# Optimization experiments

Hardware: AMD Instinct MI355X
Metric: run time of the kernel (lower is better)

Reference implementation:

```python
import jax, jax.numpy as jnp
import numpy as np

D_MODEL = 1024
NUM_HEADS = 16
HEAD_DIM = D_MODEL // NUM_HEADS


def setup_inputs() -> dict:
    key = jax.random.key(0)
    k_x, k_wqkv, k_bqkv, k_wout, k_bout = jax.random.split(key, 5)
    B, S = 2, 2048
    x = jax.random.normal(k_x, (B, S, D_MODEL), dtype=jnp.float32)
    # haiku Linear: y = x @ W + b, W shape [in, out]
    init_scale = 1.0 / np.sqrt(D_MODEL)
    W_qkv = jax.random.normal(k_wqkv, (D_MODEL, 3 * D_MODEL), dtype=jnp.float32) * init_scale
    b_qkv = jnp.zeros((3 * D_MODEL,), dtype=jnp.float32)
    W_out = jax.random.normal(k_wout, (D_MODEL, D_MODEL), dtype=jnp.float32) * init_scale
    b_out = jnp.zeros((D_MODEL,), dtype=jnp.float32)
    return {"x": x, "W_qkv": W_qkv, "b_qkv": b_qkv, "W_out": W_out, "b_out": b_out}


def reference(x, W_qkv, b_qkv, W_out, b_out):
    B, S, _ = x.shape
    qkv = x @ W_qkv + b_qkv                      # [B, S, 3*D]
    q, k, v = jnp.split(qkv, 3, axis=-1)         # each [B, S, D]
    # [B, S, D] -> [B, H, S, Hd]
    def heads(t):
        return t.reshape(B, S, NUM_HEADS, HEAD_DIM).transpose(0, 2, 1, 3)
    q, k, v = heads(q), heads(k), heads(v)
    scale = jnp.sqrt(jnp.float32(HEAD_DIM)).astype(x.dtype)
    attn = jnp.einsum('bhqd,bhkd->bhqk', q, k) / scale   # [B, H, S, S]
    attn = jax.nn.softmax(attn, axis=-1)
    out = jnp.einsum('bhqk,bhkd->bhqd', attn, v)          # [B, H, S, Hd]
    out = out.transpose(0, 2, 1, 3).reshape(B, S, D_MODEL)
    return out @ W_out + b_out
```

## Files before the change

### kernel.cpp

```cpp
#include <hip/hip_runtime.h>
#include <stdint.h>


#define BATCH 2
#define SEQ 2048
#define DM 1024
#define NH 16
#define HD 64
#define M_TOT 4096

typedef __bf16 bf16x8 __attribute__((ext_vector_type(8)));
typedef __bf16 bf16x4 __attribute__((ext_vector_type(4)));
typedef float  f32x4  __attribute__((ext_vector_type(4)));

__device__ __forceinline__ void gld_lds16(const void* g, void* l) {
    __builtin_amdgcn_global_load_lds(
        (const __attribute__((address_space(1))) uint32_t*)g,
        (__attribute__((address_space(3))) uint32_t*)l, 16, 0, 0);
}

__device__ __forceinline__ int swz(int r, int c) {
    return r * 64 + ((((c >> 3) ^ (r & 7))) << 3) + (c & 7);
}

__launch_bounds__(256)
__global__ void split_x_kernel(const float* __restrict__ x, __bf16* __restrict__ xs)
{
    const int i  = blockIdx.x * 256 + threadIdx.x;
    const int m  = i >> 8;
    const int c4 = (i & 255) * 4;
    float4 v = *reinterpret_cast<const float4*>(&x[(size_t)m * DM + c4]);
    float a[4] = {v.x, v.y, v.z, v.w};
    bf16x4 hi, lo;
    #pragma unroll
    for (int j = 0; j < 4; ++j) {
        __bf16 h = (__bf16)a[j];
        hi[j] = h;
        lo[j] = (__bf16)(a[j] - (float)h);
    }
    *reinterpret_cast<bf16x4*>(&xs[(size_t)m * (2*DM) + c4]) = hi;
    *reinterpret_cast<bf16x4*>(&xs[(size_t)m * (2*DM) + DM + c4]) = lo;
}

__launch_bounds__(256)
__global__ void split_wt_kernel(const float* __restrict__ W, __bf16* __restrict__ Wt, int N)
{
    __shared__ float T[32][33];
    const int tid = threadIdx.x;
    const int tx = tid & 31, ty = tid >> 5;
    const int k0 = blockIdx.x * 32, n0 = blockIdx.y * 32;
    #pragma unroll
    for (int i = 0; i < 4; ++i) {
        const int k = ty + 8 * i;
        T[tx][k] = W[(size_t)(k0 + k) * N + n0 + tx];
    }
    __syncthreads();
    #pragma unroll
    for (int i = 0; i < 4; ++i) {
        const int n = ty + 8 * i;
        float v = T[n][tx];
        __bf16 h = (__bf16)v;
        Wt[(size_t)(n0 + n) * (2*DM) + k0 + tx] = h;
        Wt[(size_t)(n0 + n) * (2*DM) + DM + k0 + tx] = (__bf16)(v - (float)h);
    }
}

__launch_bounds__(256)
__global__ void gemm_qkv_kernel(const __bf16* __restrict__ A,
                                const __bf16* __restrict__ Bt,
                                const float* __restrict__ bias,
                                __bf16* __restrict__ qs,
                                __bf16* __restrict__ khi_g,
                                __bf16* __restrict__ klo_g,
                                __bf16* __restrict__ vt_g)
{
    __shared__ __align__(16) __bf16 pool[18432];
    __bf16* As = pool;
    __bf16* Bs = pool + 4096;

    const int tid  = threadIdx.x;
    const int w    = tid >> 6;
    const int lane = tid & 63;
    const int n16  = lane & 15;
    const int quad = lane >> 4;
    const int bm = blockIdx.x * 128, bn = blockIdx.y * 128;
    const int wm = (w & 1) * 64,     wn = (w >> 1) * 64;

    const int srow = tid >> 2, sc = (tid & 3) * 8;
    const __bf16* Ar = A  + (size_t)(bm + srow) * (2*DM) + sc;
    const __bf16* Br = Bt + (size_t)(bn + srow) * (2*DM) + sc;

    f32x4 acc[4][4] = {};

    for (int kb = 0; kb < 3 * DM; kb += 32) {
        const int a_k = (kb < DM)     ? kb : kb - DM;
        const int b_k = (kb < 2 * DM) ? kb : kb - 2 * DM;
        __syncthreads();
        gld_lds16(Ar + a_k,                    &As[(size_t)tid * 8]);
        gld_lds16(Ar + a_k + (size_t)64*2*DM,  &As[(size_t)(256 + tid) * 8]);
        gld_lds16(Br + b_k,                    &Bs[(size_t)tid * 8]);
        gld_lds16(Br + b_k + (size_t)64*2*DM,  &Bs[(size_t)(256 + tid) * 8]);
        __syncthreads();

        bf16x8 af[4], bfr[4];
        #pragma unroll
        for (int i = 0; i < 4; ++i)
            af[i] = *reinterpret_cast<const bf16x8*>(&As[(wm + i*16 + n16) * 32 + quad * 8]);
        #pragma unroll
        for (int j = 0; j < 4; ++j)
            bfr[j] = *reinterpret_cast<const bf16x8*>(&Bs[(wn + j*16 + n16) * 32 + quad * 8]);
        #pragma unroll
        for (int i = 0; i < 4; ++i)
            #pragma unroll
            for (int j = 0; j < 4; ++j)
                acc[i][j] = __builtin_amdgcn_mfma_f32_16x16x32_bf16(af[i], bfr[j], acc[i][j], 0, 0, 0);
    }

    const int colb = bn + wn;
    const int part = colb >> 10;
    const int hh   = (colb & 1023) >> 6;
    const int brow = bm + wm;
    const int b    = brow >> 11;
    const int s0   = brow & 2047;
    const int bh   = b * NH + hh;
    const int kt   = s0 >> 6;
    const size_t tb = ((size_t)bh * 32 + kt) * 4096;

    float bv[4];
    #pragma unroll
    for (int j = 0; j < 4; ++j) bv[j] = bias[colb + j * 16 + n16];

    __bf16* scrH = pool + w * 4608;
    __bf16* scrL = scrH + 2304;
    const int lr = lane & 31, hc = lane >> 5;

    __syncthreads();

    #pragma unroll
    for (int p = 0; p < 2; ++p) {
        if (part == 2) {
            #pragma unroll
            for (int jj = 0; jj < 2; ++jj) {
                const int j = 2 * p + jj;
                #pragma unroll
                for (int i = 0; i < 4; ++i) {
                    bf16x4 v4;
                    #pragma unroll
                    for (int r = 0; r < 4; ++r)
                        v4[r] = (__bf16)(acc[i][j][r] + bv[j]);
                    *reinterpret_cast<bf16x4*>(
                        &scrH[(jj * 16 + n16) * 72 + i * 16 + quad * 4]) = v4;
                }
            }
        } else {
            #pragma unroll
            for (int ii = 0; ii < 2; ++ii) {
                const int i = 2 * p + ii;
                #pragma unroll
                for (int j = 0; j < 4; ++j) {
                    #pragma unroll
                    for (int r = 0; r < 4; ++r) {
                        float val = acc[i][j][r] + bv[j];
                        if (part == 0) val *= 0.125f;
                        __bf16 h = (__bf16)val;
                        const int so = (ii * 16 + quad * 4 + r) * 72 + j * 16 + n16;
                        scrH[so] = h;
                        scrL[so] = (__bf16)(val - (float)h);
                    }
                }
            }
        }
        __syncthreads();

        if (part == 0) {
            const size_t qbase = ((size_t)bh * SEQ + s0 + 32 * p + lr) * 128;
            #pragma unroll
            for (int t = 0; t < 4; ++t) {
                const int ch = hc * 4 + t;
                *reinterpret_cast<bf16x8*>(&qs[qbase + ch * 8]) =
                    *reinterpret_cast<const bf16x8*>(&scrH[lr * 72 + ch * 8]);
                *reinterpret_cast<bf16x8*>(&qs[qbase + 64 + ch * 8]) =
                    *reinterpret_cast<const bf16x8*>(&scrL[lr * 72 + ch * 8]);
            }
        } else if (part == 1) {
            const int kr = 32 * p + lr;
            #pragma unroll
            for (int t = 0; t < 4; ++t) {
                const int ch = hc * 4 + t;
                const int src = (ch ^ (lr & 7)) * 8;
                *reinterpret_cast<bf16x8*>(&khi_g[tb + kr * 64 + ch * 8]) =
                    *reinterpret_cast<const bf16x8*>(&scrH[lr * 72 + src]);
                *reinterpret_cast<bf16x8*>(&klo_g[tb + kr * 64 + ch * 8]) =
                    *reinterpret_cast<const bf16x8*>(&scrL[lr * 72 + src]);
            }
        } else {
            const int d = 32 * p + lr;
            #pragma unroll
            for (int t = 0; t < 4; ++t) {
                const int ch = hc * 4 + t;
                const int src = (ch ^ (lr & 7)) * 8;
                *reinterpret_cast<bf16x8*>(&vt_g[tb + d * 64 + ch * 8]) =
                    *reinterpret_cast<const bf16x8*>(&scrH[lr * 72 + src]);
            }
        }
        __syncthreads();
    }
}

__launch_bounds__(256)
__global__ void gemm_out_kernel(const __bf16* __restrict__ A,
                                const __bf16* __restrict__ Bt,
                                const float* __restrict__ bias,
                                float* __restrict__ out)
{
    __shared__ __align__(16) __bf16 As[128 * 32];
    __shared__ __align__(16) __bf16 Bs[64 * 32];

    const int tid  = threadIdx.x;
    const int w    = tid >> 6;
    const int lane = tid & 63;
    const int n16  = lane & 15;
    const int quad = lane >> 4;
    const int bm = blockIdx.x * 128, bn = blockIdx.y * 64;
    const int wm = (w & 1) * 64,     wn = (w >> 1) * 32;

    const int srow = tid >> 2, sc = (tid & 3) * 8;
    const __bf16* Ar = A  + (size_t)(bm + srow) * (2*DM) + sc;
    const __bf16* Br = Bt + (size_t)(bn + srow) * (2*DM) + sc;

    f32x4 acc[4][2] = {};

    for (int kb = 0; kb < 3 * DM; kb += 32) {
        const int a_k = (kb < DM)     ? kb : kb - DM;
        const int b_k = (kb < 2 * DM) ? kb : kb - 2 * DM;
        __syncthreads();
        gld_lds16(Ar + a_k,                    &As[(size_t)tid * 8]);
        gld_lds16(Ar + a_k + (size_t)64*2*DM,  &As[(size_t)(256 + tid) * 8]);
        gld_lds16(Br + b_k,                    &Bs[(size_t)tid * 8]);
        __syncthreads();

        bf16x8 af[4], bfr[2];
        #pragma unroll
        for (int i = 0; i < 4; ++i)
            af[i] = *reinterpret_cast<const bf16x8*>(&As[(wm + i*16 + n16) * 32 + quad * 8]);
        #pragma unroll
        for (int j = 0; j < 2; ++j)
            bfr[j] = *reinterpret_cast<const bf16x8*>(&Bs[(wn + j*16 + n16) * 32 + quad * 8]);
        #pragma unroll
        for (int i = 0; i < 4; ++i)
            #pragma unroll
            for (int j = 0; j < 2; ++j)
                acc[i][j] = __builtin_amdgcn_mfma_f32_16x16x32_bf16(af[i], bfr[j], acc[i][j], 0, 0, 0);
    }

    #pragma unroll
    for (int j = 0; j < 2; ++j) {
        const int col = bn + wn + j * 16 + n16;
        const float bvv = bias[col];
        #pragma unroll
        for (int i = 0; i < 4; ++i) {
            const int row0 = bm + wm + i * 16 + quad * 4;
            #pragma unroll
            for (int r = 0; r < 4; ++r)
                out[(size_t)(row0 + r) * DM + col] = acc[i][j][r] + bvv;
        }
    }
}

__launch_bounds__(256)
__global__ void flash_attn_dma_kernel(const __bf16* __restrict__ qs,
                                      const __bf16* __restrict__ khi_g,
                                      const __bf16* __restrict__ klo_g,
                                      const __bf16* __restrict__ vt_g,
                                      __bf16* __restrict__ ctx2)
{
    __shared__ __align__(16) __bf16 Khi[4096];
    __shared__ __align__(16) __bf16 Klo[4096];
    __shared__ __align__(16) __bf16 Vt [4096];
    __shared__ __align__(16) __bf16 Ps [4096];

    const int tid  = threadIdx.x;
    const int w    = tid >> 6;
    const int lane = tid & 63;
    const int n16  = lane & 15;
    const int quad = lane >> 4;
    const int bid  = blockIdx.x;
    const int bh = (bid & 7) * 4 + ((bid >> 3) >> 5);
    const int qt = (bid >> 3) & 31;

    const size_t qrow = ((size_t)bh * SEQ + qt * 64 + w * 16 + n16) * 128;
    bf16x8 qh[2], ql[2];
    #pragma unroll
    for (int s2 = 0; s2 < 2; ++s2) {
        qh[s2] = *reinterpret_cast<const bf16x8*>(&qs[qrow + s2 * 32 + quad * 8]);
        ql[s2] = *reinterpret_cast<const bf16x8*>(&qs[qrow + 64 + s2 * 32 + quad * 8]);
    }

    f32x4 o[4] = {};
    float m_i = -1e30f, l_i = 0.f;

    for (int kt = 0; kt < 32; ++kt) {
        const size_t tb = ((size_t)bh * 32 + kt) * 4096;
        __syncthreads();
        #pragma unroll
        for (int t = 0; t < 6; ++t) {
            const int ch = w * 6 + t;
            const int arr = ch >> 3, sub = ch & 7;
            const int eo = sub * 512 + lane * 8;
            const __bf16* g = (arr == 0 ? khi_g : arr == 1 ? klo_g : vt_g) + tb + eo;
            __bf16* l = (arr == 0 ? Khi : arr == 1 ? Klo : Vt) + eo;
            gld_lds16(g, l);
        }
        __syncthreads();

        f32x4 st[4] = {};
        #pragma unroll
        for (int kg = 0; kg < 4; ++kg) {
            const int r = kg * 16 + n16;
            #pragma unroll
            for (int s2 = 0; s2 < 2; ++s2) {
                const int off = r * 64 + (((s2 * 4 + quad) ^ (r & 7)) << 3);
                bf16x8 kh = *reinterpret_cast<const bf16x8*>(&Khi[off]);
                bf16x8 kl = *reinterpret_cast<const bf16x8*>(&Klo[off]);
                st[kg] = __builtin_amdgcn_mfma_f32_16x16x32_bf16(kh, qh[s2], st[kg], 0, 0, 0);
                st[kg] = __builtin_amdgcn_mfma_f32_16x16x32_bf16(kh, ql[s2], st[kg], 0, 0, 0);
                st[kg] = __builtin_amdgcn_mfma_f32_16x16x32_bf16(kl, qh[s2], st[kg], 0, 0, 0);
            }
        }

        float mx = st[0][0];
        #pragma unroll
        for (int kg = 0; kg < 4; ++kg)
            #pragma unroll
            for (int r2 = 0; r2 < 4; ++r2)
                mx = fmaxf(mx, st[kg][r2]);
        mx = fmaxf(mx, __shfl_xor(mx, 16, 64));
        mx = fmaxf(mx, __shfl_xor(mx, 32, 64));
        const float mnew = fmaxf(m_i, mx);
        const float alpha = __expf(m_i - mnew);
        m_i = mnew;
        float rs = 0.f;
        #pragma unroll
        for (int kg = 0; kg < 4; ++kg)
            #pragma unroll
            for (int r2 = 0; r2 < 4; ++r2) {
                float pp = __expf(st[kg][r2] - mnew);
                st[kg][r2] = pp;
                rs += pp;
            }
        rs += __shfl_xor(rs, 16, 64);
        rs += __shfl_xor(rs, 32, 64);
        l_i = l_i * alpha + rs;

        const int prow = w * 16 + n16;
        #pragma unroll
        for (int kg = 0; kg < 4; ++kg)
            #pragma unroll
            for (int r2 = 0; r2 < 4; ++r2)
                Ps[swz(prow, kg * 16 + quad * 4 + r2)] = (__bf16)st[kg][r2];

        #pragma unroll
        for (int r2 = 0; r2 < 4; ++r2) {
            const float a = __shfl(alpha, (quad << 4) + quad * 4 + r2, 64);
            #pragma unroll
            for (int c = 0; c < 4; ++c)
                o[c][r2] *= a;
        }

        bf16x8 pa[2];
        #pragma unroll
        for (int s2 = 0; s2 < 2; ++s2)
            pa[s2] = *reinterpret_cast<const bf16x8*>(
                &Ps[prow * 64 + (((s2 * 4 + quad) ^ (n16 & 7)) << 3)]);
        #pragma unroll
        for (int c = 0; c < 4; ++c) {
            const int vr = c * 16 + n16;
            #pragma unroll
            for (int s2 = 0; s2 < 2; ++s2) {
                bf16x8 vb = *reinterpret_cast<const bf16x8*>(
                    &Vt[vr * 64 + (((s2 * 4 + quad) ^ (vr & 7)) << 3)]);
                o[c] = __builtin_amdgcn_mfma_f32_16x16x32_bf16(pa[s2], vb, o[c], 0, 0, 0);
            }
        }
    }

    const int b = bh >> 4, hh = bh & 15;
    #pragma unroll
    for (int r2 = 0; r2 < 4; ++r2) {
        const float l = __shfl(l_i, (quad << 4) + quad * 4 + r2, 64);
        const float linv = 1.0f / l;
        const int srow = qt * 64 + w * 16 + quad * 4 + r2;
        const size_t rowoff = (size_t)(b * SEQ + srow) * (2*DM);
        #pragma unroll
        for (int c = 0; c < 4; ++c) {
            const int col = hh * HD + c * 16 + n16;
            float v = o[c][r2] * linv;
            __bf16 h = (__bf16)v;
            ctx2[rowoff + col] = h;
            ctx2[rowoff + DM + col] = (__bf16)(v - (float)h);
        }
    }
}

extern "C" void kernel_launch(void* const* d_in, const int* in_sizes, int n_in,
                              void* d_out, int out_size, void* d_ws, size_t ws_size,
                              hipStream_t stream)
{
    const float* x    = (const float*)d_in[0];
    const float* Wqkv = (const float*)d_in[1];
    const float* bqkv = (const float*)d_in[2];
    const float* Wout = (const float*)d_in[3];
    const float* bout = (const float*)d_in[4];
    float* out = (float*)d_out;

    char* ws = (char*)d_ws;
    __bf16* xs   = (__bf16*)(ws);
    __bf16* ctx2 = xs;
    __bf16* wqt  = (__bf16*)(ws + (size_t)16 * 1024 * 1024);
    __bf16* wot  = (__bf16*)(ws + (size_t)28 * 1024 * 1024);
    __bf16* qsb  = (__bf16*)(ws + (size_t)32 * 1024 * 1024);
    __bf16* khi  = (__bf16*)(ws + (size_t)48 * 1024 * 1024);
    __bf16* klo  = (__bf16*)(ws + (size_t)56 * 1024 * 1024);
    __bf16* vt   = (__bf16*)(ws + (size_t)64 * 1024 * 1024);

    split_x_kernel<<<dim3(M_TOT * (DM / 4) / 256), 256, 0, stream>>>(x, xs);
    split_wt_kernel<<<dim3(DM / 32, (3 * DM) / 32), 256, 0, stream>>>(Wqkv, wqt, 3 * DM);
    split_wt_kernel<<<dim3(DM / 32, DM / 32), 256, 0, stream>>>(Wout, wot, DM);

    gemm_qkv_kernel<<<dim3(M_TOT / 128, (3 * DM) / 128), 256, 0, stream>>>(
        xs, wqt, bqkv, qsb, khi, klo, vt);
    flash_attn_dma_kernel<<<dim3(1024), 256, 0, stream>>>(qsb, khi, klo, vt, ctx2);
    gemm_out_kernel<<<dim3(M_TOT / 128, DM / 64), 256, 0, stream>>>(
        ctx2, wot, bout, out);
}
```

Baseline: 323.0 us.

## Double attention query tile per block, use exp2 softmax, vectorize weight split

Flash attention blocks now run 8 waves over 128 query rows, so each K/V tile staged in LDS serves twice as many queries and the global-to-LDS traffic per query halves. The softmax uses exp2 with log2(e) folded into the Q scale, and P is stored to LDS as 4-element vectors instead of scalars. The weight split/transpose kernel uses 64x64 tiles with float4 loads and 16-byte stores. Larger blocks reduce the grid to 512 blocks, which may lower latency hiding per CU.

```diff
diff --git a/kernel.cpp b/kernel.cpp
--- a/kernel.cpp
+++ b/kernel.cpp
@@ -8,6 +8,7 @@
 #define NH 16
 #define HD 64
 #define M_TOT 4096
+#define QSCALE 0.18033688011112042f
 
 typedef __bf16 bf16x8 __attribute__((ext_vector_type(8)));
 typedef __bf16 bf16x4 __attribute__((ext_vector_type(4)));
@@ -45,23 +46,35 @@
 __launch_bounds__(256)
 __global__ void split_wt_kernel(const float* __restrict__ W, __bf16* __restrict__ Wt, int N)
 {
-    __shared__ float T[32][33];
+    __shared__ float T[64][69];
     const int tid = threadIdx.x;
-    const int tx = tid & 31, ty = tid >> 5;
-    const int k0 = blockIdx.x * 32, n0 = blockIdx.y * 32;
-    #pragma unroll
-    for (int i = 0; i < 4; ++i) {
-        const int k = ty + 8 * i;
-        T[tx][k] = W[(size_t)(k0 + k) * N + n0 + tx];
+    const int k0 = blockIdx.x * 64, n0 = blockIdx.y * 64;
+
+    {
+        const int kr = tid >> 4, c4 = (tid & 15) * 4;
+        #pragma unroll
+        for (int i = 0; i < 4; ++i) {
+            float4 v = *reinterpret_cast<const float4*>(
+                &W[(size_t)(k0 + kr + 16 * i) * N + n0 + c4]);
+            *reinterpret_cast<float4*>(&T[kr + 16 * i][c4]) = v;
+        }
     }
     __syncthreads();
-    #pragma unroll
-    for (int i = 0; i < 4; ++i) {
-        const int n = ty + 8 * i;
-        float v = T[n][tx];
-        __bf16 h = (__bf16)v;
-        Wt[(size_t)(n0 + n) * (2*DM) + k0 + tx] = h;
-        Wt[(size_t)(n0 + n) * (2*DM) + DM + k0 + tx] = (__bf16)(v - (float)h);
+    {
+        const int n = tid >> 2, kc = (tid & 3) * 16;
+        __bf16 hi[16], lo[16];
+        #pragma unroll
+        for (int j = 0; j < 16; ++j) {
+            float v = T[kc + j][n];
+            __bf16 h = (__bf16)v;
+            hi[j] = h;
+            lo[j] = (__bf16)(v - (float)h);
+        }
+        const size_t ro = (size_t)(n0 + n) * (2*DM) + k0 + kc;
+        *reinterpret_cast<bf16x8*>(&Wt[ro])          = *reinterpret_cast<bf16x8*>(&hi[0]);
+        *reinterpret_cast<bf16x8*>(&Wt[ro + 8])      = *reinterpret_cast<bf16x8*>(&hi[8]);
+        *reinterpret_cast<bf16x8*>(&Wt[ro + DM])     = *reinterpret_cast<bf16x8*>(&lo[0]);
+        *reinterpret_cast<bf16x8*>(&Wt[ro + DM + 8]) = *reinterpret_cast<bf16x8*>(&lo[8]);
     }
 }
 
@@ -161,7 +174,7 @@
                     #pragma unroll
                     for (int r = 0; r < 4; ++r) {
                         float val = acc[i][j][r] + bv[j];
-                        if (part == 0) val *= 0.125f;
+                        if (part == 0) val *= QSCALE;
                         __bf16 h = (__bf16)val;
                         const int so = (ii * 16 + quad * 4 + r) * 72 + j * 16 + n16;
                         scrH[so] = h;
@@ -267,7 +280,7 @@
     }
 }
 
-__launch_bounds__(256)
+__launch_bounds__(512)
 __global__ void flash_attn_dma_kernel(const __bf16* __restrict__ qs,
                                       const __bf16* __restrict__ khi_g,
                                       const __bf16* __restrict__ klo_g,
@@ -277,7 +290,7 @@
     __shared__ __align__(16) __bf16 Khi[4096];
     __shared__ __align__(16) __bf16 Klo[4096];
     __shared__ __align__(16) __bf16 Vt [4096];
-    __shared__ __align__(16) __bf16 Ps [4096];
+    __shared__ __align__(16) __bf16 Ps [8192];
 
     const int tid  = threadIdx.x;
     const int w    = tid >> 6;
@@ -285,10 +298,10 @@
     const int n16  = lane & 15;
     const int quad = lane >> 4;
     const int bid  = blockIdx.x;
-    const int bh = (bid & 7) * 4 + ((bid >> 3) >> 5);
-    const int qt = (bid >> 3) & 31;
-
-    const size_t qrow = ((size_t)bh * SEQ + qt * 64 + w * 16 + n16) * 128;
+    const int bh = (bid & 7) * 4 + (bid >> 7);
+    const int qt = (bid >> 3) & 15;
+
+    const size_t qrow = ((size_t)bh * SEQ + qt * 128 + w * 16 + n16) * 128;
     bf16x8 qh[2], ql[2];
     #pragma unroll
     for (int s2 = 0; s2 < 2; ++s2) {
@@ -299,12 +312,14 @@
     f32x4 o[4] = {};
     float m_i = -1e30f, l_i = 0.f;
 
+    const int prow = w * 16 + n16;
+
     for (int kt = 0; kt < 32; ++kt) {
         const size_t tb = ((size_t)bh * 32 + kt) * 4096;
         __syncthreads();
         #pragma unroll
-        for (int t = 0; t < 6; ++t) {
-            const int ch = w * 6 + t;
+        for (int t = 0; t < 3; ++t) {
+            const int ch = w * 3 + t;
             const int arr = ch >> 3, sub = ch & 7;
             const int eo = sub * 512 + lane * 8;
             const __bf16* g = (arr == 0 ? khi_g : arr == 1 ? klo_g : vt_g) + tb + eo;
@@ -337,14 +352,14 @@
         mx = fmaxf(mx, __shfl_xor(mx, 16, 64));
         mx = fmaxf(mx, __shfl_xor(mx, 32, 64));
         const float mnew = fmaxf(m_i, mx);
-        const float alpha = __expf(m_i - mnew);
+        const float alpha = exp2f(m_i - mnew);
         m_i = mnew;
         float rs = 0.f;
         #pragma unroll
         for (int kg = 0; kg < 4; ++kg)
             #pragma unroll
             for (int r2 = 0; r2 < 4; ++r2) {
-                float pp = __expf(st[kg][r2] - mnew);
+                float pp = exp2f(st[kg][r2] - mnew);
                 st[kg][r2] = pp;
                 rs += pp;
             }
@@ -352,12 +367,15 @@
         rs += __shfl_xor(rs, 32, 64);
         l_i = l_i * alpha + rs;
 
-        const int prow = w * 16 + n16;
-        #pragma unroll
-        for (int kg = 0; kg < 4; ++kg)
-            #pragma unroll
-            for (int r2 = 0; r2 < 4; ++r2)
-                Ps[swz(prow, kg * 16 + quad * 4 + r2)] = (__bf16)st[kg][r2];
+        #pragma unroll
+        for (int kg = 0; kg < 4; ++kg) {
+            bf16x4 p4;
+            #pragma unroll
+            for (int r2 = 0; r2 < 4; ++r2) p4[r2] = (__bf16)st[kg][r2];
+            const int ch = kg * 2 + (quad >> 1);
+            const int off = prow * 64 + ((ch ^ (prow & 7)) << 3) + (quad & 1) * 4;
+            *reinterpret_cast<bf16x4*>(&Ps[off]) = p4;
+        }
 
         #pragma unroll
         for (int r2 = 0; r2 < 4; ++r2) {
@@ -371,7 +389,7 @@
         #pragma unroll
         for (int s2 = 0; s2 < 2; ++s2)
             pa[s2] = *reinterpret_cast<const bf16x8*>(
-                &Ps[prow * 64 + (((s2 * 4 + quad) ^ (n16 & 7)) << 3)]);
+                &Ps[prow * 64 + (((s2 * 4 + quad) ^ (prow & 7)) << 3)]);
         #pragma unroll
         for (int c = 0; c < 4; ++c) {
             const int vr = c * 16 + n16;
@@ -389,7 +407,7 @@
     for (int r2 = 0; r2 < 4; ++r2) {
         const float l = __shfl(l_i, (quad << 4) + quad * 4 + r2, 64);
         const float linv = 1.0f / l;
-        const int srow = qt * 64 + w * 16 + quad * 4 + r2;
+        const int srow = qt * 128 + w * 16 + quad * 4 + r2;
         const size_t rowoff = (size_t)(b * SEQ + srow) * (2*DM);
         #pragma unroll
         for (int c = 0; c < 4; ++c) {
@@ -424,12 +442,12 @@
     __bf16* vt   = (__bf16*)(ws + (size_t)64 * 1024 * 1024);
 
     split_x_kernel<<<dim3(M_TOT * (DM / 4) / 256), 256, 0, stream>>>(x, xs);
-    split_wt_kernel<<<dim3(DM / 32, (3 * DM) / 32), 256, 0, stream>>>(Wqkv, wqt, 3 * DM);
-    split_wt_kernel<<<dim3(DM / 32, DM / 32), 256, 0, stream>>>(Wout, wot, DM);
+    split_wt_kernel<<<dim3(DM / 64, (3 * DM) / 64), 256, 0, stream>>>(Wqkv, wqt, 3 * DM);
+    split_wt_kernel<<<dim3(DM / 64, DM / 64), 256, 0, stream>>>(Wout, wot, DM);
 
     gemm_qkv_kernel<<<dim3(M_TOT / 128, (3 * DM) / 128), 256, 0, stream>>>(
         xs, wqt, bqkv, qsb, khi, klo, vt);
-    flash_attn_dma_kernel<<<dim3(1024), 256, 0, stream>>>(qsb, khi, klo, vt, ctx2);
+    flash_attn_dma_kernel<<<dim3(512), 512, 0, stream>>>(qsb, khi, klo, vt, ctx2);
     gemm_out_kernel<<<dim3(M_TOT / 128, DM / 64), 256, 0, stream>>>(
         ctx2, wot, bout, out);
 }
```

Result: no change. 319.7 us (-1.0%).
